# Optimization experiments

Hardware: AMD Instinct MI355X
Metric: run time of the kernel (lower is better)

The kernel has to match this reference:

```python
import jax, jax.numpy as jnp
import numpy as np

B, L, D_MODEL, H = 2, 2048, 1024, 16
D_K = D_MODEL // H


def entmax15(z):
    """Exact 1.5-entmax along last axis (Peters et al. 2019, sort-based)."""
    z = z - jnp.max(z, axis=-1, keepdims=True)
    z = z / 2.0
    K = z.shape[-1]
    z_sorted = -jnp.sort(-z, axis=-1)  # descending
    kk = jnp.arange(1, K + 1, dtype=z.dtype)
    cs = jnp.cumsum(z_sorted, axis=-1)
    cs2 = jnp.cumsum(z_sorted * z_sorted, axis=-1)
    mean = cs / kk
    ss = cs2 - cs * mean                 # k * (E[z^2] - E[z]^2)
    delta = (1.0 - ss) / kk
    tau = mean - jnp.sqrt(jnp.clip(delta, 0.0))
    support = jnp.sum((tau <= z_sorted).astype(jnp.int32), axis=-1, keepdims=True)
    tau_star = jnp.take_along_axis(tau, support - 1, axis=-1)
    p = jnp.clip(z - tau_star, 0.0)
    return p * p


def setup_inputs() -> dict:
    key = jax.random.key(0)
    ks = jax.random.split(key, 8)
    s = 1.0 / np.sqrt(D_MODEL)
    return {
        "q": jax.random.normal(ks[0], (B, L, D_MODEL), jnp.float32),
        "k": jax.random.normal(ks[1], (B, L, D_MODEL), jnp.float32),
        "v": jax.random.normal(ks[2], (B, L, D_MODEL), jnp.float32),
        "mask": jnp.ones((B, L, L), jnp.int32),
        "w_q": jax.random.normal(ks[3], (D_MODEL, D_MODEL), jnp.float32) * s,
        "w_k": jax.random.normal(ks[4], (D_MODEL, D_MODEL), jnp.float32) * s,
        "w_v": jax.random.normal(ks[5], (D_MODEL, D_MODEL), jnp.float32) * s,
        "w_o": jax.random.normal(ks[6], (D_MODEL, D_MODEL), jnp.float32) * s,
    }


def reference(q, k, v, mask, w_q, w_k, w_v, w_o):
    b, l, _ = q.shape
    # torch Linear (no bias): y = x @ W^T
    def proj(x, w):
        return jnp.einsum('bld,ed->ble', x, w).reshape(b, l, H, D_K).transpose(0, 2, 1, 3)
    Q, K, V = proj(q, w_q), proj(k, w_k), proj(v, w_v)  # [B,H,L,d_k]
    scores = jnp.einsum('bhqd,bhkd->bhqk', Q, K) / np.sqrt(D_K)
    scores = jnp.where(mask[:, None, :, :] == 0, jnp.finfo(scores.dtype).min, scores)
    probs = entmax15(scores)
    out = jnp.einsum('bhqk,bhkd->bhqd', probs, V)
    out = out.transpose(0, 2, 1, 3).reshape(b, l, D_MODEL)
    return jnp.einsum('bld,ed->ble', out, w_o)
```

## Files before the change

kernel.cpp:

```cpp
#include <hip/hip_runtime.h>


typedef _Float16 f16;
typedef __attribute__((ext_vector_type(8))) _Float16 f16x8;
typedef __attribute__((ext_vector_type(4))) _Float16 f16x4;
typedef __attribute__((ext_vector_type(2))) _Float16 f16x2;
typedef __attribute__((ext_vector_type(4))) float f32x4;
typedef unsigned int u32;

static __device__ __forceinline__ f16x2 max2(f16x2 a, f16x2 b) {
    return __builtin_elementwise_max(a, b);
}

static __device__ __forceinline__ f16x2 shfl2(f16x2 v, int off) {
    union { f16x2 h; int i; } u;
    u.h = v;
    u.i = __shfl_xor(u.i, off);
    return u.h;
}

static __device__ __forceinline__ f16x2 pkrtz(float a, float b) {
    union { __fp16 __attribute__((ext_vector_type(2))) p; f16x2 h; } u;
    u.p = __builtin_amdgcn_cvt_pkrtz(a, b);
    return u.h;
}

__global__ __launch_bounds__(256)
void pack_mask(const int* __restrict__ mask, u32* __restrict__ bits)
{
    int idx = blockIdx.x * 256 + threadIdx.x;
    const int4* p = (const int4*)&mask[(size_t)idx * 32];
    u32 v = 0;
#pragma unroll
    for (int i = 0; i < 8; i++) {
        int4 m = p[i];
        if (m.x != 0) v |= 1u << (i * 4 + 0);
        if (m.y != 0) v |= 1u << (i * 4 + 1);
        if (m.z != 0) v |= 1u << (i * 4 + 2);
        if (m.w != 0) v |= 1u << (i * 4 + 3);
    }
    const int wd = idx & 63;
    const int q = (idx >> 6) & 2047;
    const int b = idx >> 17;
    bits[(((size_t)(b * 128 + (q >> 4)) * 8 + (wd >> 3)) << 7) + ((q & 15) << 3) + (wd & 7)] = v;
}

__global__ __launch_bounds__(512)
void gemm_qkv(const float* __restrict__ Aq, const float* __restrict__ Ak,
              const float* __restrict__ Av, const float* __restrict__ W0,
              const float* __restrict__ W1, const float* __restrict__ W2,
              f16* __restrict__ Qp, f16* __restrict__ Kp, f16* __restrict__ Vp)
{
    __shared__ __align__(16) f16 As[128 * 40];
    __shared__ __align__(16) f16 Bs[128 * 40];

    const int tid = threadIdx.x;
    const int wsel = blockIdx.y >> 3;
    const float* A  = wsel == 0 ? Aq : (wsel == 1 ? Ak : Av);
    const float* Wp = wsel == 0 ? W0 : (wsel == 1 ? W1 : W2);
    const int mBase = blockIdx.x * 128;
    const int nBase = (blockIdx.y & 7) * 128;

    const int lane = tid & 63, w = tid >> 6;
    const int g = lane >> 4, c = lane & 15;
    const int wm = w >> 1, wn = w & 1;

    const int sr = tid >> 2;
    const int sq = tid & 3;

    f32x4 acc[2][4];
    const f32x4 vzero = {0.f, 0.f, 0.f, 0.f};
#pragma unroll
    for (int i = 0; i < 2; i++)
#pragma unroll
        for (int j = 0; j < 4; j++) acc[i][j] = vzero;

    for (int k0 = 0; k0 < 1024; k0 += 32) {
        __syncthreads();
        {
            const float4* p = (const float4*)&A[(size_t)(mBase + sr) * 1024 + k0 + sq * 8];
            float4 x0 = p[0], x1 = p[1];
            f16x8 av;
            av[0] = (f16)x0.x; av[1] = (f16)x0.y; av[2] = (f16)x0.z; av[3] = (f16)x0.w;
            av[4] = (f16)x1.x; av[5] = (f16)x1.y; av[6] = (f16)x1.z; av[7] = (f16)x1.w;
            *(f16x8*)&As[sr * 40 + sq * 8] = av;

            const float4* pw = (const float4*)&Wp[(size_t)(nBase + sr) * 1024 + k0 + sq * 8];
            float4 w0 = pw[0], w1 = pw[1];
            f16x8 bv;
            bv[0] = (f16)w0.x; bv[1] = (f16)w0.y; bv[2] = (f16)w0.z; bv[3] = (f16)w0.w;
            bv[4] = (f16)w1.x; bv[5] = (f16)w1.y; bv[6] = (f16)w1.z; bv[7] = (f16)w1.w;
            *(f16x8*)&Bs[sr * 40 + sq * 8] = bv;
        }
        __syncthreads();

        f16x8 af[2], bf[4];
#pragma unroll
        for (int mt = 0; mt < 2; mt++)
            af[mt] = *(const f16x8*)&As[(wm * 32 + mt * 16 + c) * 40 + g * 8];
#pragma unroll
        for (int nt = 0; nt < 4; nt++)
            bf[nt] = *(const f16x8*)&Bs[(wn * 64 + nt * 16 + c) * 40 + g * 8];
#pragma unroll
        for (int mt = 0; mt < 2; mt++)
#pragma unroll
            for (int nt = 0; nt < 4; nt++)
                acc[mt][nt] = __builtin_amdgcn_mfma_f32_16x16x32_f16(af[mt], bf[nt], acc[mt][nt], 0, 0, 0);
    }

#pragma unroll
    for (int mt = 0; mt < 2; mt++)
#pragma unroll
        for (int nt = 0; nt < 4; nt++) {
            int row0 = mBase + wm * 32 + mt * 16 + g * 4;
            int col = nBase + wn * 64 + nt * 16 + c;
            if (wsel == 2) {
                int b = row0 >> 11, l0 = row0 & 2047;
                int h = col >> 6, dk = col & 63;
                int bh = b * 16 + h;
                int t = l0 >> 4, gv = (l0 & 15) >> 2;
                int nd = dk >> 4, c16 = dk & 15;
                f16x4 pv;
#pragma unroll
                for (int r = 0; r < 4; r++) pv[r] = (f16)acc[mt][nt][r];
                *(f16x4*)&Vp[(size_t)(bh * 128 + t) * 1024 + nd * 256 + c16 * 16 + gv * 4] = pv;
            } else {
                f16* Cp = wsel == 0 ? Qp : Kp;
                const float scale = wsel == 0 ? 0.0625f : 1.0f;
#pragma unroll
                for (int r = 0; r < 4; r++) {
                    int row = row0 + r;
                    float v = acc[mt][nt][r] * scale;
                    int b = row >> 11, l = row & 2047;
                    int h = col >> 6, dk = col & 63;
                    int bh = b * 16 + h;
                    int t = l >> 4, ck = l & 15;
                    int half = dk >> 5, gk = (dk >> 3) & 3, e = dk & 7;
                    Cp[((size_t)(bh * 128 + t) * 2 + half) * 512 + ck * 32 + gk * 8 + e] = (f16)v;
                }
            }
        }
}

__global__ __launch_bounds__(512)
void gemm_out(const f16* __restrict__ Ap, const float* __restrict__ Wp,
              float* __restrict__ Cp)
{
    __shared__ __align__(16) f16 As[128 * 40];
    __shared__ __align__(16) f16 Bs[128 * 40];

    const int tid = threadIdx.x;
    const int mBase = blockIdx.x * 128;
    const int nBase = blockIdx.y * 128;

    const int lane = tid & 63, w = tid >> 6;
    const int g = lane >> 4, c = lane & 15;
    const int wm = w >> 1, wn = w & 1;

    const int sr = tid >> 2;
    const int sq = tid & 3;

    f32x4 acc[2][4];
    const f32x4 vzero = {0.f, 0.f, 0.f, 0.f};
#pragma unroll
    for (int i = 0; i < 2; i++)
#pragma unroll
        for (int j = 0; j < 4; j++) acc[i][j] = vzero;

    for (int k0 = 0; k0 < 1024; k0 += 32) {
        __syncthreads();
        {
            *(f16x8*)&As[sr * 40 + sq * 8] =
                *(const f16x8*)&Ap[(size_t)(mBase + sr) * 1024 + k0 + sq * 8];

            const float4* pw = (const float4*)&Wp[(size_t)(nBase + sr) * 1024 + k0 + sq * 8];
            float4 w0 = pw[0], w1 = pw[1];
            f16x8 bv;
            bv[0] = (f16)w0.x; bv[1] = (f16)w0.y; bv[2] = (f16)w0.z; bv[3] = (f16)w0.w;
            bv[4] = (f16)w1.x; bv[5] = (f16)w1.y; bv[6] = (f16)w1.z; bv[7] = (f16)w1.w;
            *(f16x8*)&Bs[sr * 40 + sq * 8] = bv;
        }
        __syncthreads();

        f16x8 af[2], bf[4];
#pragma unroll
        for (int mt = 0; mt < 2; mt++)
            af[mt] = *(const f16x8*)&As[(wm * 32 + mt * 16 + c) * 40 + g * 8];
#pragma unroll
        for (int nt = 0; nt < 4; nt++)
            bf[nt] = *(const f16x8*)&Bs[(wn * 64 + nt * 16 + c) * 40 + g * 8];
#pragma unroll
        for (int mt = 0; mt < 2; mt++)
#pragma unroll
            for (int nt = 0; nt < 4; nt++)
                acc[mt][nt] = __builtin_amdgcn_mfma_f32_16x16x32_f16(af[mt], bf[nt], acc[mt][nt], 0, 0, 0);
    }

#pragma unroll
    for (int mt = 0; mt < 2; mt++)
#pragma unroll
        for (int nt = 0; nt < 4; nt++) {
            int row0 = mBase + wm * 32 + mt * 16 + g * 4;
            int col = nBase + wn * 64 + nt * 16 + c;
#pragma unroll
            for (int r = 0; r < 4; r++)
                Cp[(size_t)(row0 + r) * 1024 + col] = acc[mt][nt][r];
        }
}

__global__ __launch_bounds__(512, 4)
void attn_entmax(const f16* __restrict__ Qp, const f16* __restrict__ Kp,
                 const f16* __restrict__ Vp, const u32* __restrict__ Mp,
                 f16* __restrict__ AO)
{
    constexpr int CAP = 512;
    constexpr int BSTR = 513;
    __shared__ __align__(16) char LB[8 * 16 * 68 * 4];
    __shared__ int cntS[16];
    __shared__ float redM[8][16];
    __shared__ float redN[2][8][16][2];
    __shared__ float tau2s[16], zmaxs[16], taus[16];

    float* bucket = (float*)LB;
    float* Ored = (float*)LB;

    const int tid = threadIdx.x;
    const int w = tid >> 6, lane = tid & 63;
    const int g = lane >> 4, c = lane & 15;

    const int bid = blockIdx.x;
    const int q8 = bid >> 3;
    const int bh = (bid & 7) * 4 + (q8 >> 7);
    const int qt = q8 & 127;
    const int qb = qt * 16;
    const int b = bh >> 4, h = bh & 15;

    if (tid < 16) cntS[tid] = 0;

    const f16* qbase = &Qp[(size_t)(bh * 128 + qt) * 1024 + c * 32 + g * 8];
    f16x8 bq0 = *(const f16x8*)qbase;
    f16x8 bq1 = *(const f16x8*)(qbase + 512);

    const u32* mbase = &Mp[(((size_t)(b * 128 + qt) * 8 + w) << 7) + (c << 3)];
    uint4 mA = *(const uint4*)mbase;
    uint4 mB = *(const uint4*)(mbase + 4);
    u32 mb[8] = {mA.x, mA.y, mA.z, mA.w, mB.x, mB.y, mB.z, mB.w};

    f16x2 hS[32];
    f16x2 rmax; rmax.x = (f16)(-30000.f); rmax.y = (f16)(-30000.f);
    const f32x4 vz = {0.f, 0.f, 0.f, 0.f};
    const f16* kbaseP = &Kp[(size_t)(bh * 128 + w * 16) * 1024 + c * 32 + g * 8];

    f16x8 kb[2][8];
#pragma unroll
    for (int i = 0; i < 4; i++) {
        const f16* kp = kbaseP + (size_t)i * 1024;
        kb[0][2 * i]     = *(const f16x8*)kp;
        kb[0][2 * i + 1] = *(const f16x8*)(kp + 512);
    }
#pragma unroll
    for (int ch = 0; ch < 4; ch++) {
        if (ch < 3) {
#pragma unroll
            for (int i = 0; i < 4; i++) {
                const f16* kp = kbaseP + (size_t)((ch + 1) * 4 + i) * 1024;
                kb[(ch + 1) & 1][2 * i]     = *(const f16x8*)kp;
                kb[(ch + 1) & 1][2 * i + 1] = *(const f16x8*)(kp + 512);
            }
        }
#pragma unroll
        for (int i = 0; i < 4; i++) {
            const int t = ch * 4 + i;
            f32x4 z = __builtin_amdgcn_mfma_f32_16x16x32_f16(kb[ch & 1][2 * i], bq0, vz, 0, 0, 0);
            z = __builtin_amdgcn_mfma_f32_16x16x32_f16(kb[ch & 1][2 * i + 1], bq1, z, 0, 0, 0);
            u32 mw = mb[t >> 1];
            if (__builtin_expect(mw != 0xFFFFFFFFu, 0)) {
                u32 b4 = mw >> ((t & 1) * 16 + g * 4);
#pragma unroll
                for (int r = 0; r < 4; r++)
                    if (!((b4 >> r) & 1)) z[r] = -30000.f;
            }
            f16x2 p0 = pkrtz(z[0], z[1]);
            f16x2 p1 = pkrtz(z[2], z[3]);
            hS[2 * t] = p0;
            hS[2 * t + 1] = p1;
            rmax = max2(rmax, max2(p0, p1));
        }
    }

    float zx = fmaxf((float)rmax.x, (float)rmax.y);
    zx = fmaxf(zx, __shfl_xor(zx, 16));
    zx = fmaxf(zx, __shfl_xor(zx, 32));
    if (lane < 16) redM[w][c] = zx;
    __syncthreads();
    float zmax = -3e38f;
#pragma unroll
    for (int ww = 0; ww < 8; ww++) zmax = fmaxf(zmax, redM[ww][c]);

    f16x2 zero2; zero2.x = (f16)0.f; zero2.y = (f16)0.f;
    float tau = zmax - 1.0f;
    int buf = 0;
#pragma unroll 1
    for (int it = 0; it < 2; ++it) {
        f16 tn = (f16)tau;
        f16x2 tv; tv.x = tn; tv.y = tn;
        f16x2 s1p = zero2, s2p = zero2;
#pragma unroll
        for (int i = 0; i < 32; i++) {
            f16x2 d = max2(hS[i] - tv, zero2);
            s1p = s1p + d;
            s2p = s2p + d * d;
        }
        s1p = s1p + shfl2(s1p, 16);
        s2p = s2p + shfl2(s2p, 16);
        s1p = s1p + shfl2(s1p, 32);
        s2p = s2p + shfl2(s2p, 32);
        float s1 = (float)s1p.x + (float)s1p.y;
        float s2 = (float)s2p.x + (float)s2p.y;
        if (lane < 16) { redN[buf][w][c][0] = s1; redN[buf][w][c][1] = s2; }
        __syncthreads();
        float a = 0.f, f = 0.f;
#pragma unroll
        for (int ww = 0; ww < 8; ww++) {
            float2 v2 = *(const float2*)&redN[buf][ww][c][0];
            a += v2.x; f += v2.y;
        }
        if (a > 1e-9f)
            tau = fminf(tau + (f - 1.0f) / (2.0f * a), zmax - 1e-3f);
        buf ^= 1;
    }
    if (w == 0 && lane < 16) { tau2s[c] = tau; zmaxs[c] = zmax; }

    const f16 thrh = (f16)(tau - 0.02f);
    f16x2 thr2; thr2.x = thrh; thr2.y = thrh;
#pragma unroll
    for (int i = 0; i < 32; i++) {
        union { f16x2 h; u32 u; } dd;
        dd.h = hS[i] - thr2;
        u32 pos = ~dd.u & 0x80008000u;
        if (__builtin_expect(pos != 0, 0)) {
            if (hS[i].x > thrh) { int id = atomicAdd(&cntS[c], 1); if (id < CAP) bucket[c * BSTR + id] = (float)hS[i].x; }
            if (hS[i].y > thrh) { int id = atomicAdd(&cntS[c], 1); if (id < CAP) bucket[c * BSTR + id] = (float)hS[i].y; }
        }
    }
    __syncthreads();

    {
        const int qi = 4 * w + (lane >> 4);
        const int sl = lane & 15;
        const int cnt = min(cntS[qi], CAP);
        const int ns = (cnt + 15) >> 4;
        float tq = tau2s[qi];
        const float zq = zmaxs[qi];
#pragma unroll 1
        for (int it = 0; it < 4; ++it) {
            float s1 = 0.f, s2 = 0.f;
#pragma unroll 1
            for (int s = 0; s < ns; s++) {
                int i = sl + 16 * s;
                float v = (i < cnt) ? bucket[qi * BSTR + i] : -1e30f;
                float d = fmaxf(v - tq, 0.f);
                s1 += d; s2 = fmaf(d, d, s2);
            }
#pragma unroll
            for (int off = 1; off <= 8; off <<= 1) {
                s1 += __shfl_xor(s1, off);
                s2 += __shfl_xor(s2, off);
            }
            if (s1 > 1e-12f) tq = fminf(tq + (s2 - 1.0f) / (2.0f * s1), zq - 1e-3f);
        }
#pragma unroll 1
        for (int rf = 0; rf < 3; ++rf) {
            float kc = 0.f, s1 = 0.f, s2 = 0.f;
#pragma unroll 1
            for (int s = 0; s < ns; s++) {
                int i = sl + 16 * s;
                float v = (i < cnt) ? bucket[qi * BSTR + i] : -1e30f;
                float d = v - tq;
                if (d > 0.f) { kc += 1.f; s1 += d; s2 = fmaf(d, d, s2); }
            }
#pragma unroll
            for (int off = 1; off <= 8; off <<= 1) {
                kc += __shfl_xor(kc, off);
                s1 += __shfl_xor(s1, off);
                s2 += __shfl_xor(s2, off);
            }
            float K_ = fmaxf(kc, 1.0f);
            float disc = fmaxf(s1 * s1 - K_ * (s2 - 1.0f), 0.f);
            tq += (s1 - sqrtf(disc)) / K_;
        }
        if (sl == 0) taus[qi] = tq;
    }
    __syncthreads();

    const f16 tch = (f16)taus[c];
    f16x2 tv2; tv2.x = tch; tv2.y = tch;
    f32x4 O[4];
#pragma unroll
    for (int nd = 0; nd < 4; nd++) O[nd] = vz;
    const f16* vbase = &Vp[(size_t)(bh * 128 + w * 16) * 1024 + c * 16 + g * 4];
#pragma unroll
    for (int t = 0; t < 16; t++) {
        f16x2 da = max2(hS[2 * t] - tv2, zero2);
        f16x2 db = max2(hS[2 * t + 1] - tv2, zero2);
        da = da * da;
        db = db * db;
        union { f16x4 v4; f16x2 h2[2]; } pu;
        pu.h2[0] = da; pu.h2[1] = db;
        const f16* vp = vbase + (size_t)t * 1024;
#pragma unroll
        for (int nd = 0; nd < 4; nd++) {
            f16x4 va = *(const f16x4*)(vp + nd * 256);
            O[nd] = __builtin_amdgcn_mfma_f32_16x16x16f16(va, pu.v4, O[nd], 0, 0, 0);
        }
    }

#pragma unroll
    for (int nd = 0; nd < 4; nd++)
        *(f32x4*)&Ored[(w * 16 + c) * 68 + nd * 16 + g * 4] = O[nd];
    __syncthreads();

    const int qrow = tid >> 5;
    const int dp = tid & 31;
    float o0 = 0.f, o1 = 0.f;
#pragma unroll
    for (int ww = 0; ww < 8; ww++) {
        float2 v = *(const float2*)&Ored[(ww * 16 + qrow) * 68 + dp * 2];
        o0 += v.x; o1 += v.y;
    }
    f16x2 pk = pkrtz(o0, o1);
    *(f16x2*)&AO[(size_t)(b * 2048 + qb + qrow) * 1024 + h * 64 + dp * 2] = pk;
}

extern "C" void kernel_launch(void* const* d_in, const int* in_sizes, int n_in,
                              void* d_out, int out_size, void* d_ws, size_t ws_size,
                              hipStream_t stream)
{
    const float* q  = (const float*)d_in[0];
    const float* k  = (const float*)d_in[1];
    const float* v  = (const float*)d_in[2];
    const int* mask = (const int*)d_in[3];
    const float* wq = (const float*)d_in[4];
    const float* wk = (const float*)d_in[5];
    const float* wv = (const float*)d_in[6];
    const float* wo = (const float*)d_in[7];

    char* ws = (char*)d_ws;
    const size_t SZ = 8388608ull;
    f16* Qb  = (f16*)(ws);
    f16* Kb  = (f16*)(ws + SZ);
    f16* Vb  = (f16*)(ws + 2 * SZ);
    f16* AOb = (f16*)(ws + 3 * SZ);
    u32* Mb  = (u32*)(ws + 4 * SZ);

    pack_mask<<<1024, 256, 0, stream>>>(mask, Mb);
    gemm_qkv<<<dim3(32, 24), 512, 0, stream>>>(q, k, v, wq, wk, wv, Qb, Kb, Vb);
    attn_entmax<<<4096, 512, 0, stream>>>(Qb, Kb, Vb, Mb, AOb);
    gemm_out<<<dim3(32, 8), 512, 0, stream>>>(AOb, wo, (float*)d_out);
}
```

Before: 376.3 us.

## Process two 16-query tiles per attention block to reuse K and V loads

Each attention block now handles 32 query rows as two 16-row sub-tiles (A and B) that share the same K and V fragments. Global K/V traffic per query is halved, and the grid is halved to match. The cost is twice the score registers per thread, which forces launch bounds down to 2 blocks per SM and lowers occupancy. The explicit K double-buffer prefetch is dropped in favour of direct per-step loads, which may expose load latency. Shared-memory buffers and the final reduction are widened to 32 rows, with a vectorized fp16x4 output store.

Result: faster. 336.4 us (median of 2 runs) (-10.6%).

```diff
diff --git a/kernel.cpp b/kernel.cpp
--- a/kernel.cpp
+++ b/kernel.cpp
@@ -208,18 +208,18 @@
         }
 }
 
-__global__ __launch_bounds__(512, 4)
+__global__ __launch_bounds__(512, 2)
 void attn_entmax(const f16* __restrict__ Qp, const f16* __restrict__ Kp,
                  const f16* __restrict__ Vp, const u32* __restrict__ Mp,
                  f16* __restrict__ AO)
 {
     constexpr int CAP = 512;
     constexpr int BSTR = 513;
-    __shared__ __align__(16) char LB[8 * 16 * 68 * 4];
-    __shared__ int cntS[16];
-    __shared__ float redM[8][16];
-    __shared__ float redN[2][8][16][2];
-    __shared__ float tau2s[16], zmaxs[16], taus[16];
+    __shared__ __align__(16) char LB[8 * 32 * 68 * 4];
+    __shared__ int cntS[32];
+    __shared__ float redM[8][32];
+    __shared__ float redN[2][8][32][2];
+    __shared__ float tau2s[32], zmaxs[32], taus[32];
 
     float* bucket = (float*)LB;
     float* Ored = (float*)LB;
@@ -229,118 +229,140 @@
     const int g = lane >> 4, c = lane & 15;
 
     const int bid = blockIdx.x;
-    const int q8 = bid >> 3;
-    const int bh = (bid & 7) * 4 + (q8 >> 7);
-    const int qt = q8 & 127;
-    const int qb = qt * 16;
+    const int q6 = bid >> 3;
+    const int bh = (bid & 7) * 4 + (q6 >> 6);
+    const int qt = q6 & 63;
+    const int qb = qt * 32;
     const int b = bh >> 4, h = bh & 15;
 
-    if (tid < 16) cntS[tid] = 0;
-
-    const f16* qbase = &Qp[(size_t)(bh * 128 + qt) * 1024 + c * 32 + g * 8];
-    f16x8 bq0 = *(const f16x8*)qbase;
-    f16x8 bq1 = *(const f16x8*)(qbase + 512);
-
-    const u32* mbase = &Mp[(((size_t)(b * 128 + qt) * 8 + w) << 7) + (c << 3)];
-    uint4 mA = *(const uint4*)mbase;
-    uint4 mB = *(const uint4*)(mbase + 4);
-    u32 mb[8] = {mA.x, mA.y, mA.z, mA.w, mB.x, mB.y, mB.z, mB.w};
-
-    f16x2 hS[32];
-    f16x2 rmax; rmax.x = (f16)(-30000.f); rmax.y = (f16)(-30000.f);
+    if (tid < 32) cntS[tid] = 0;
+
+    const f16* qbaseA = &Qp[(size_t)(bh * 128 + 2 * qt) * 1024 + c * 32 + g * 8];
+    f16x8 bqA0 = *(const f16x8*)qbaseA;
+    f16x8 bqA1 = *(const f16x8*)(qbaseA + 512);
+    f16x8 bqB0 = *(const f16x8*)(qbaseA + 1024);
+    f16x8 bqB1 = *(const f16x8*)(qbaseA + 1536);
+
+    const u32* mbaseA = &Mp[(((size_t)(b * 128 + 2 * qt) * 8 + w) << 7) + (c << 3)];
+    uint4 mA0 = *(const uint4*)mbaseA;
+    uint4 mA1 = *(const uint4*)(mbaseA + 4);
+    uint4 mB0 = *(const uint4*)(mbaseA + 128);
+    uint4 mB1 = *(const uint4*)(mbaseA + 132);
+    u32 mbA[8] = {mA0.x, mA0.y, mA0.z, mA0.w, mA1.x, mA1.y, mA1.z, mA1.w};
+    u32 mbB[8] = {mB0.x, mB0.y, mB0.z, mB0.w, mB1.x, mB1.y, mB1.z, mB1.w};
+
+    f16x2 hSA[32], hSB[32];
+    f16x2 rmaxA; rmaxA.x = (f16)(-30000.f); rmaxA.y = (f16)(-30000.f);
+    f16x2 rmaxB = rmaxA;
     const f32x4 vz = {0.f, 0.f, 0.f, 0.f};
     const f16* kbaseP = &Kp[(size_t)(bh * 128 + w * 16) * 1024 + c * 32 + g * 8];
-
-    f16x8 kb[2][8];
-#pragma unroll
-    for (int i = 0; i < 4; i++) {
-        const f16* kp = kbaseP + (size_t)i * 1024;
-        kb[0][2 * i]     = *(const f16x8*)kp;
-        kb[0][2 * i + 1] = *(const f16x8*)(kp + 512);
-    }
-#pragma unroll
-    for (int ch = 0; ch < 4; ch++) {
-        if (ch < 3) {
-#pragma unroll
-            for (int i = 0; i < 4; i++) {
-                const f16* kp = kbaseP + (size_t)((ch + 1) * 4 + i) * 1024;
-                kb[(ch + 1) & 1][2 * i]     = *(const f16x8*)kp;
-                kb[(ch + 1) & 1][2 * i + 1] = *(const f16x8*)(kp + 512);
-            }
-        }
-#pragma unroll
-        for (int i = 0; i < 4; i++) {
-            const int t = ch * 4 + i;
-            f32x4 z = __builtin_amdgcn_mfma_f32_16x16x32_f16(kb[ch & 1][2 * i], bq0, vz, 0, 0, 0);
-            z = __builtin_amdgcn_mfma_f32_16x16x32_f16(kb[ch & 1][2 * i + 1], bq1, z, 0, 0, 0);
-            u32 mw = mb[t >> 1];
-            if (__builtin_expect(mw != 0xFFFFFFFFu, 0)) {
-                u32 b4 = mw >> ((t & 1) * 16 + g * 4);
-#pragma unroll
-                for (int r = 0; r < 4; r++)
-                    if (!((b4 >> r) & 1)) z[r] = -30000.f;
-            }
-            f16x2 p0 = pkrtz(z[0], z[1]);
-            f16x2 p1 = pkrtz(z[2], z[3]);
-            hS[2 * t] = p0;
-            hS[2 * t + 1] = p1;
-            rmax = max2(rmax, max2(p0, p1));
-        }
-    }
-
-    float zx = fmaxf((float)rmax.x, (float)rmax.y);
-    zx = fmaxf(zx, __shfl_xor(zx, 16));
-    zx = fmaxf(zx, __shfl_xor(zx, 32));
-    if (lane < 16) redM[w][c] = zx;
+#pragma unroll
+    for (int t = 0; t < 16; t++) {
+        const f16* kp = kbaseP + (size_t)t * 1024;
+        f16x8 ka0 = *(const f16x8*)kp;
+        f16x8 ka1 = *(const f16x8*)(kp + 512);
+        f32x4 zA = __builtin_amdgcn_mfma_f32_16x16x32_f16(ka0, bqA0, vz, 0, 0, 0);
+        zA = __builtin_amdgcn_mfma_f32_16x16x32_f16(ka1, bqA1, zA, 0, 0, 0);
+        f32x4 zB = __builtin_amdgcn_mfma_f32_16x16x32_f16(ka0, bqB0, vz, 0, 0, 0);
+        zB = __builtin_amdgcn_mfma_f32_16x16x32_f16(ka1, bqB1, zB, 0, 0, 0);
+        u32 mwA = mbA[t >> 1], mwB = mbB[t >> 1];
+        if (__builtin_expect(mwA != 0xFFFFFFFFu, 0)) {
+            u32 b4 = mwA >> ((t & 1) * 16 + g * 4);
+#pragma unroll
+            for (int r = 0; r < 4; r++)
+                if (!((b4 >> r) & 1)) zA[r] = -30000.f;
+        }
+        if (__builtin_expect(mwB != 0xFFFFFFFFu, 0)) {
+            u32 b4 = mwB >> ((t & 1) * 16 + g * 4);
+#pragma unroll
+            for (int r = 0; r < 4; r++)
+                if (!((b4 >> r) & 1)) zB[r] = -30000.f;
+        }
+        f16x2 a0 = pkrtz(zA[0], zA[1]), a1 = pkrtz(zA[2], zA[3]);
+        f16x2 b0 = pkrtz(zB[0], zB[1]), b1 = pkrtz(zB[2], zB[3]);
+        hSA[2 * t] = a0; hSA[2 * t + 1] = a1;
+        hSB[2 * t] = b0; hSB[2 * t + 1] = b1;
+        rmaxA = max2(rmaxA, max2(a0, a1));
+        rmaxB = max2(rmaxB, max2(b0, b1));
+    }
+
+    float zxA = fmaxf((float)rmaxA.x, (float)rmaxA.y);
+    float zxB = fmaxf((float)rmaxB.x, (float)rmaxB.y);
+    zxA = fmaxf(zxA, __shfl_xor(zxA, 16)); zxA = fmaxf(zxA, __shfl_xor(zxA, 32));
+    zxB = fmaxf(zxB, __shfl_xor(zxB, 16)); zxB = fmaxf(zxB, __shfl_xor(zxB, 32));
+    if (lane < 16) { redM[w][c] = zxA; redM[w][16 + c] = zxB; }
     __syncthreads();
-    float zmax = -3e38f;
-#pragma unroll
-    for (int ww = 0; ww < 8; ww++) zmax = fmaxf(zmax, redM[ww][c]);
+    float zmaxA = -3e38f, zmaxB = -3e38f;
+#pragma unroll
+    for (int ww = 0; ww < 8; ww++) {
+        zmaxA = fmaxf(zmaxA, redM[ww][c]);
+        zmaxB = fmaxf(zmaxB, redM[ww][16 + c]);
+    }
 
     f16x2 zero2; zero2.x = (f16)0.f; zero2.y = (f16)0.f;
-    float tau = zmax - 1.0f;
+    float tauA = zmaxA - 1.0f, tauB = zmaxB - 1.0f;
     int buf = 0;
 #pragma unroll 1
     for (int it = 0; it < 2; ++it) {
-        f16 tn = (f16)tau;
-        f16x2 tv; tv.x = tn; tv.y = tn;
-        f16x2 s1p = zero2, s2p = zero2;
+        f16 tnA = (f16)tauA, tnB = (f16)tauB;
+        f16x2 tvA; tvA.x = tnA; tvA.y = tnA;
+        f16x2 tvB; tvB.x = tnB; tvB.y = tnB;
+        f16x2 s1A = zero2, s2A = zero2, s1B = zero2, s2B = zero2;
 #pragma unroll
         for (int i = 0; i < 32; i++) {
-            f16x2 d = max2(hS[i] - tv, zero2);
-            s1p = s1p + d;
-            s2p = s2p + d * d;
-        }
-        s1p = s1p + shfl2(s1p, 16);
-        s2p = s2p + shfl2(s2p, 16);
-        s1p = s1p + shfl2(s1p, 32);
-        s2p = s2p + shfl2(s2p, 32);
-        float s1 = (float)s1p.x + (float)s1p.y;
-        float s2 = (float)s2p.x + (float)s2p.y;
-        if (lane < 16) { redN[buf][w][c][0] = s1; redN[buf][w][c][1] = s2; }
+            f16x2 dA = max2(hSA[i] - tvA, zero2);
+            f16x2 dB = max2(hSB[i] - tvB, zero2);
+            s1A = s1A + dA; s2A = s2A + dA * dA;
+            s1B = s1B + dB; s2B = s2B + dB * dB;
+        }
+        s1A = s1A + shfl2(s1A, 16); s2A = s2A + shfl2(s2A, 16);
+        s1A = s1A + shfl2(s1A, 32); s2A = s2A + shfl2(s2A, 32);
+        s1B = s1B + shfl2(s1B, 16); s2B = s2B + shfl2(s2B, 16);
+        s1B = s1B + shfl2(s1B, 32); s2B = s2B + shfl2(s2B, 32);
+        float a1 = (float)s1A.x + (float)s1A.y;
+        float f1 = (float)s2A.x + (float)s2A.y;
+        float a2 = (float)s1B.x + (float)s1B.y;
+        float f2 = (float)s2B.x + (float)s2B.y;
+        if (lane < 16) {
+            redN[buf][w][c][0] = a1; redN[buf][w][c][1] = f1;
+            redN[buf][w][16 + c][0] = a2; redN[buf][w][16 + c][1] = f2;
+        }
         __syncthreads();
-        float a = 0.f, f = 0.f;
+        float aA = 0.f, fA = 0.f, aB = 0.f, fB = 0.f;
 #pragma unroll
         for (int ww = 0; ww < 8; ww++) {
-            float2 v2 = *(const float2*)&redN[buf][ww][c][0];
-            a += v2.x; f += v2.y;
-        }
-        if (a > 1e-9f)
-            tau = fminf(tau + (f - 1.0f) / (2.0f * a), zmax - 1e-3f);
+            float2 vA = *(const float2*)&redN[buf][ww][c][0];
+            float2 vB = *(const float2*)&redN[buf][ww][16 + c][0];
+            aA += vA.x; fA += vA.y;
+            aB += vB.x; fB += vB.y;
+        }
+        if (aA > 1e-9f) tauA = fminf(tauA + (fA - 1.0f) / (2.0f * aA), zmaxA - 1e-3f);
+        if (aB > 1e-9f) tauB = fminf(tauB + (fB - 1.0f) / (2.0f * aB), zmaxB - 1e-3f);
         buf ^= 1;
     }
-    if (w == 0 && lane < 16) { tau2s[c] = tau; zmaxs[c] = zmax; }
-
-    const f16 thrh = (f16)(tau - 0.02f);
-    f16x2 thr2; thr2.x = thrh; thr2.y = thrh;
+    if (w == 0 && lane < 16) {
+        tau2s[c] = tauA; tau2s[16 + c] = tauB;
+        zmaxs[c] = zmaxA; zmaxs[16 + c] = zmaxB;
+    }
+
+    const f16 thrA = (f16)(tauA - 0.02f);
+    const f16 thrB = (f16)(tauB - 0.02f);
+    f16x2 thrA2; thrA2.x = thrA; thrA2.y = thrA;
+    f16x2 thrB2; thrB2.x = thrB; thrB2.y = thrB;
 #pragma unroll
     for (int i = 0; i < 32; i++) {
-        union { f16x2 h; u32 u; } dd;
-        dd.h = hS[i] - thr2;
-        u32 pos = ~dd.u & 0x80008000u;
-        if (__builtin_expect(pos != 0, 0)) {
-            if (hS[i].x > thrh) { int id = atomicAdd(&cntS[c], 1); if (id < CAP) bucket[c * BSTR + id] = (float)hS[i].x; }
-            if (hS[i].y > thrh) { int id = atomicAdd(&cntS[c], 1); if (id < CAP) bucket[c * BSTR + id] = (float)hS[i].y; }
+        union { f16x2 h; u32 u; } dA, dB;
+        dA.h = hSA[i] - thrA2;
+        dB.h = hSB[i] - thrB2;
+        u32 posA = ~dA.u & 0x80008000u;
+        u32 posB = ~dB.u & 0x80008000u;
+        if (__builtin_expect(posA != 0, 0)) {
+            if (hSA[i].x > thrA) { int id = atomicAdd(&cntS[c], 1); if (id < CAP) bucket[c * BSTR + id] = (float)hSA[i].x; }
+            if (hSA[i].y > thrA) { int id = atomicAdd(&cntS[c], 1); if (id < CAP) bucket[c * BSTR + id] = (float)hSA[i].y; }
+        }
+        if (__builtin_expect(posB != 0, 0)) {
+            if (hSB[i].x > thrB) { int id = atomicAdd(&cntS[16 + c], 1); if (id < CAP) bucket[(16 + c) * BSTR + id] = (float)hSB[i].x; }
+            if (hSB[i].y > thrB) { int id = atomicAdd(&cntS[16 + c], 1); if (id < CAP) bucket[(16 + c) * BSTR + id] = (float)hSB[i].y; }
         }
     }
     __syncthreads();
@@ -393,43 +415,52 @@
     }
     __syncthreads();
 
-    const f16 tch = (f16)taus[c];
-    f16x2 tv2; tv2.x = tch; tv2.y = tch;
-    f32x4 O[4];
-#pragma unroll
-    for (int nd = 0; nd < 4; nd++) O[nd] = vz;
+    const f16 tcA = (f16)taus[c];
+    const f16 tcB = (f16)taus[16 + c];
+    f16x2 tvA2; tvA2.x = tcA; tvA2.y = tcA;
+    f16x2 tvB2; tvB2.x = tcB; tvB2.y = tcB;
+    f32x4 O0[4], O1[4];
+#pragma unroll
+    for (int nd = 0; nd < 4; nd++) { O0[nd] = vz; O1[nd] = vz; }
     const f16* vbase = &Vp[(size_t)(bh * 128 + w * 16) * 1024 + c * 16 + g * 4];
 #pragma unroll
     for (int t = 0; t < 16; t++) {
-        f16x2 da = max2(hS[2 * t] - tv2, zero2);
-        f16x2 db = max2(hS[2 * t + 1] - tv2, zero2);
-        da = da * da;
-        db = db * db;
-        union { f16x4 v4; f16x2 h2[2]; } pu;
-        pu.h2[0] = da; pu.h2[1] = db;
+        f16x2 daA = max2(hSA[2 * t] - tvA2, zero2);
+        f16x2 dbA = max2(hSA[2 * t + 1] - tvA2, zero2);
+        f16x2 daB = max2(hSB[2 * t] - tvB2, zero2);
+        f16x2 dbB = max2(hSB[2 * t + 1] - tvB2, zero2);
+        daA = daA * daA; dbA = dbA * dbA;
+        daB = daB * daB; dbB = dbB * dbB;
+        union { f16x4 v4; f16x2 h2[2]; } puA, puB;
+        puA.h2[0] = daA; puA.h2[1] = dbA;
+        puB.h2[0] = daB; puB.h2[1] = dbB;
         const f16* vp = vbase + (size_t)t * 1024;
 #pragma unroll
         for (int nd = 0; nd < 4; nd++) {
             f16x4 va = *(const f16x4*)(vp + nd * 256);
-            O[nd] = __builtin_amdgcn_mfma_f32_16x16x16f16(va, pu.v4, O[nd], 0, 0, 0);
-        }
-    }
-
-#pragma unroll
-    for (int nd = 0; nd < 4; nd++)
-        *(f32x4*)&Ored[(w * 16 + c) * 68 + nd * 16 + g * 4] = O[nd];
+            O0[nd] = __builtin_amdgcn_mfma_f32_16x16x16f16(va, puA.v4, O0[nd], 0, 0, 0);
+            O1[nd] = __builtin_amdgcn_mfma_f32_16x16x16f16(va, puB.v4, O1[nd], 0, 0, 0);
+        }
+    }
+
+#pragma unroll
+    for (int nd = 0; nd < 4; nd++) {
+        *(f32x4*)&Ored[(w * 32 + c) * 68 + nd * 16 + g * 4] = O0[nd];
+        *(f32x4*)&Ored[(w * 32 + 16 + c) * 68 + nd * 16 + g * 4] = O1[nd];
+    }
     __syncthreads();
 
-    const int qrow = tid >> 5;
-    const int dp = tid & 31;
-    float o0 = 0.f, o1 = 0.f;
+    const int qr = tid >> 4;
+    const int d0 = (tid & 15) * 4;
+    float4 accv = {0.f, 0.f, 0.f, 0.f};
 #pragma unroll
     for (int ww = 0; ww < 8; ww++) {
-        float2 v = *(const float2*)&Ored[(ww * 16 + qrow) * 68 + dp * 2];
-        o0 += v.x; o1 += v.y;
-    }
-    f16x2 pk = pkrtz(o0, o1);
-    *(f16x2*)&AO[(size_t)(b * 2048 + qb + qrow) * 1024 + h * 64 + dp * 2] = pk;
+        float4 v = *(const float4*)&Ored[(ww * 32 + qr) * 68 + d0];
+        accv.x += v.x; accv.y += v.y; accv.z += v.z; accv.w += v.w;
+    }
+    f16x4 pk;
+    pk[0] = (f16)accv.x; pk[1] = (f16)accv.y; pk[2] = (f16)accv.z; pk[3] = (f16)accv.w;
+    *(f16x4*)&AO[(size_t)(b * 2048 + qb + qr) * 1024 + h * 64 + d0] = pk;
 }
 
 extern "C" void kernel_launch(void* const* d_in, const int* in_sizes, int n_in,
@@ -455,6 +486,6 @@
 
     pack_mask<<<1024, 256, 0, stream>>>(mask, Mb);
     gemm_qkv<<<dim3(32, 24), 512, 0, stream>>>(q, k, v, wq, wk, wv, Qb, Kb, Vb);
-    attn_entmax<<<4096, 512, 0, stream>>>(Qb, Kb, Vb, Mb, AOb);
+    attn_entmax<<<2048, 512, 0, stream>>>(Qb, Kb, Vb, Mb, AOb);
     gemm_out<<<dim3(32, 8), 512, 0, stream>>>(AOb, wo, (float*)d_out);
 }
```
